# Optimization experiments

Hardware: AMD Instinct MI355X
Metric: run time of the kernel (lower is better)

## Reference

```python
import jax, jax.numpy as jnp
import numpy as np

QMIN, QMAX = -128.0, 127.0

@jax.custom_vjp
def ste_round(x):
    return jnp.round(x)

def _ste_fwd(x):
    return jnp.round(x), None

def _ste_bwd(_, g):
    return (g,)

ste_round.defvjp(_ste_fwd, _ste_bwd)

def fake_quant_act(x, scale):
    # Int8 per-tensor fake quant: q = clip(round(x/s)) * s
    return jnp.clip(ste_round(x / scale), QMIN, QMAX) * scale

def fake_quant_weight(w):
    # Int8WeightPerTensorFloat: scale from max-abs statistic
    s = jnp.max(jnp.abs(w)) / QMAX
    return jnp.clip(ste_round(w / s), QMIN, QMAX) * s

def conv2d(x, w, b, pad):
    y = jax.lax.conv_general_dilated(
        x, w, window_strides=(1, 1), padding=[(pad, pad), (pad, pad)],
        dimension_numbers=('NCHW', 'OIHW', 'NCHW'))
    return y + b[None, :, None, None]

def maxpool2(x):
    return jax.lax.reduce_window(
        x, -jnp.inf, jax.lax.max, (1, 1, 2, 2), (1, 1, 2, 2), 'VALID')

def setup_inputs() -> dict:
    key = jax.random.key(0)
    ks = jax.random.split(key, 12)
    def w_init(k, shape, fan_in):
        return jax.random.normal(k, shape, jnp.float32) * (1.0 / np.sqrt(fan_in))
    inp = {
        'x': jax.random.normal(ks[0], (32, 1, 256, 256), jnp.float32),
        'w1': w_init(ks[1], (16, 1, 3, 3), 1 * 9),
        'b1': jax.random.normal(ks[2], (16,), jnp.float32) * 0.01,
        'w2': w_init(ks[3], (32, 16, 3, 3), 16 * 9),
        'b2': jax.random.normal(ks[4], (32,), jnp.float32) * 0.01,
        'w3': w_init(ks[5], (32, 32, 5, 5), 32 * 25),
        'b3': jax.random.normal(ks[6], (32,), jnp.float32) * 0.01,
        'w4': w_init(ks[7], (16, 32, 3, 3), 32 * 9),
        'b4': jax.random.normal(ks[8], (16,), jnp.float32) * 0.01,
        'wc': w_init(ks[9], (10, 16), 16),
        'bc': jax.random.normal(ks[10], (10,), jnp.float32) * 0.01,
        # 11 learned per-tensor activation scales, kept strictly positive
        'act_scales': jax.random.uniform(ks[11], (11,), jnp.float32) * 0.05 + 0.01,
    }
    return inp

def reference(x, w1, b1, w2, b2, w3, b3, w4, b4, wc, bc, act_scales):
    s = act_scales
    x = fake_quant_act(x, s[0])                                  # input_quant
    x = conv2d(x, fake_quant_weight(w1), b1, 0)                  # conv1 (3x3, p0)
    x = fake_quant_act(jax.nn.relu(x), s[1])                     # relu1
    x = fake_quant_act(x, s[2])                                  # quant1
    x = conv2d(x, fake_quant_weight(w2), b2, 1)                  # conv2 (3x3, p1)
    x = fake_quant_act(jax.nn.relu(x), s[3])                     # relu2
    x = fake_quant_act(x, s[4])                                  # quant2
    x = conv2d(x, fake_quant_weight(w3), b3, 2)                  # conv3 (5x5, p2)
    x = fake_quant_act(jax.nn.relu(x), s[5])                     # relu3
    x = fake_quant_act(x, s[6])                                  # quant3
    x = maxpool2(x)                                              # pool1
    x = fake_quant_act(x, s[7])                                  # pool1_quant
    x = conv2d(x, fake_quant_weight(w4), b4, 0)                  # conv4 (3x3, p0)
    x = fake_quant_act(jax.nn.relu(x), s[8])                     # relu4
    x = fake_quant_act(x, s[9])                                  # quant4
    x = jnp.mean(x, axis=(2, 3))                                 # global avg pool -> [B,16]
    x = fake_quant_act(x, s[10])                                 # pool_quant
    return x @ fake_quant_weight(wc).T + bc                      # classifier -> [B,10]
```

## Files before the change

### kernel.cpp

```cpp
#include <hip/hip_runtime.h>
#include <math.h>


typedef int i32x4  __attribute__((ext_vector_type(4)));
typedef int i32x16 __attribute__((ext_vector_type(16)));

__device__ __forceinline__ int quant_clip(float v) {
  float r = rintf(v);
  r = fminf(fmaxf(r, -128.0f), 127.0f);
  return (int)r;
}

__device__ __forceinline__ int pack4i8(int q0, int q1, int q2, int q3) {
  return (q0 & 255) | ((q1 & 255) << 8) | ((q2 & 255) << 16) | ((q3 & 255) << 24);
}

__global__ __launch_bounds__(256) void k_quant_weights(
    const float* __restrict__ w1, const float* __restrict__ w2,
    const float* __restrict__ w3, const float* __restrict__ w4,
    const float* __restrict__ wc, float* __restrict__ wscale,
    int* __restrict__ qw1, int* __restrict__ qw2B, int* __restrict__ qw3B,
    int* __restrict__ qw4B, int* __restrict__ qwc)
{
  __shared__ float red[256];
  __shared__ float ssh;
  const int t = blockIdx.x, tid = threadIdx.x;
  const float* src = (t == 0) ? w1 : (t == 1) ? w2 : (t == 2) ? w3 : (t == 3) ? w4 : wc;
  const int nsrc   = (t == 0) ? 144 : (t == 1) ? 4608 : (t == 2) ? 25600 : (t == 3) ? 4608 : 160;

  float m = 0.0f;
  for (int i = tid; i < nsrc; i += 256) m = fmaxf(m, fabsf(src[i]));
  red[tid] = m;
  __syncthreads();
  for (int s = 128; s > 0; s >>= 1) {
    if (tid < s) red[tid] = fmaxf(red[tid], red[tid + s]);
    __syncthreads();
  }
  if (tid == 0) { ssh = red[0] / 127.0f; wscale[t] = ssh; }
  __syncthreads();
  const float s = ssh;

  if (t == 0) {
    for (int i = tid; i < 144; i += 256) qw1[i] = quant_clip(w1[i] / s);
  } else if (t == 1) {
    for (int wi = tid; wi < 1536; wi += 256) {
      int step = wi >> 8, rem = wi & 255;
      int ln = rem >> 2, w = rem & 3;
      int oc = ln & 31, h = ln >> 5;
      int ky = step >> 1, kxp = (step & 1) * 2;
      int q[4];
      #pragma unroll
      for (int j = 0; j < 4; j++) {
        int k = h * 16 + w * 4 + j;
        int ic = k & 15, kx = kxp + (k >> 4);
        float val = (kx < 3) ? w2[((oc * 16 + ic) * 3 + ky) * 3 + kx] : 0.0f;
        q[j] = quant_clip(val / s);
      }
      qw2B[wi] = pack4i8(q[0], q[1], q[2], q[3]);
    }
  } else if (t == 2) {
    for (int wi = tid; wi < 6400; wi += 256) {
      int tap = wi >> 8, rem = wi & 255;
      int ln = rem >> 2, w = rem & 3;
      int oc = ln & 31, h = ln >> 5;
      int ky = tap / 5, kx = tap % 5;
      int q[4];
      #pragma unroll
      for (int j = 0; j < 4; j++) {
        int ic = h * 16 + w * 4 + j;
        q[j] = quant_clip(w3[((oc * 32 + ic) * 5 + ky) * 5 + kx] / s);
      }
      qw3B[wi] = pack4i8(q[0], q[1], q[2], q[3]);
    }
  } else if (t == 3) {
    for (int wi = tid; wi < 1280; wi += 256) {
      int mf = wi >> 8, rem = wi & 255;
      int ln = rem >> 2, w = rem & 3;
      int oc = ln & 15, chunk = ln >> 4;
      int tp = 2 * mf + (chunk >> 1);
      int half = chunk & 1;
      int q[4];
      #pragma unroll
      for (int j = 0; j < 4; j++) {
        float val = 0.0f;
        if (tp < 9) {
          int ky = tp / 3, kx = tp % 3;
          int ic = half * 16 + w * 4 + j;
          val = w4[((oc * 32 + ic) * 3 + ky) * 3 + kx];
        }
        q[j] = quant_clip(val / s);
      }
      qw4B[wi] = pack4i8(q[0], q[1], q[2], q[3]);
    }
  } else {
    for (int wi = tid; wi < 40; wi += 256) {
      int o = wi / 4, i4 = wi % 4;
      int q[4];
      #pragma unroll
      for (int j = 0; j < 4; j++) q[j] = quant_clip(wc[o * 16 + i4 * 4 + j] / s);
      qwc[wi] = pack4i8(q[0], q[1], q[2], q[3]);
    }
  }
}

__global__ __launch_bounds__(256) void k_quant_input(
    const float* __restrict__ x, const float* __restrict__ scales,
    int* __restrict__ q0w)
{
  int i = blockIdx.x * 256 + threadIdx.x;
  if (i >= 524288) return;
  float inv = 1.0f / scales[0];
  float4 v = ((const float4*)x)[i];
  q0w[i] = pack4i8(quant_clip(v.x * inv), quant_clip(v.y * inv),
                   quant_clip(v.z * inv), quant_clip(v.w * inv));
}

__global__ __launch_bounds__(256) void k_zero_border(int* __restrict__ a2p)
{
  int i = blockIdx.x * 256 + threadIdx.x;
  int n = i >> 11, p = i & 2047;
  int row, col;
  if (p < 1032) {
    int rb = p / 258;
    row = (rb < 2) ? rb : 254 + rb;
    col = p % 258;
  } else {
    int q = p - 1032;
    int cb = q & 3;
    col = (cb < 2) ? cb : 254 + cb;
    row = 2 + (q >> 2);
  }
  int4* dst = (int4*)(a2p + (((size_t)n * 258 + row) * 258 + col) * 8);
  dst[0] = make_int4(0, 0, 0, 0);
  dst[1] = make_int4(0, 0, 0, 0);
}

__global__ __launch_bounds__(256) void k_conv1(
    const signed char* __restrict__ q0, const int* __restrict__ qw1,
    const float* __restrict__ b1, const float* __restrict__ scales,
    const float* __restrict__ wscale, int* __restrict__ a1)
{
  __shared__ int wsh[144];
  __shared__ signed char lut[128];
  if (threadIdx.x < 144) wsh[threadIdx.x] = qw1[threadIdx.x];
  if (threadIdx.x < 128) {
    float s1 = scales[1], inv2 = 1.0f / scales[2];
    lut[threadIdx.x] =
        (signed char)(int)fminf(rintf(((float)threadIdx.x * s1) * inv2), 127.0f);
  }
  __syncthreads();

  int pix = blockIdx.x * 256 + threadIdx.x;
  const int TOT = 32 * 254 * 254;
  if (pix >= TOT) return;
  int n = pix / (254 * 254), r = pix % (254 * 254);
  int oy = r / 254, ox = r % 254;

  int av[9];
  const signed char* base = q0 + (n * 256 + oy) * 256 + ox;
  #pragma unroll
  for (int ky = 0; ky < 3; ky++)
    #pragma unroll
    for (int kx = 0; kx < 3; kx++)
      av[ky * 3 + kx] = (int)base[ky * 256 + kx];

  float inv1 = 1.0f / scales[1];
  float scl = scales[0] * wscale[0];
  int outw[4];
  #pragma unroll
  for (int g = 0; g < 4; g++) {
    int q[4];
    #pragma unroll
    for (int j = 0; j < 4; j++) {
      int oc = g * 4 + j;
      int acc = 0;
      #pragma unroll
      for (int k = 0; k < 9; k++) acc += av[k] * wsh[oc * 9 + k];
      float y = fmaf(scl, (float)acc, b1[oc]);
      int idx = (int)fminf(fmaxf(rintf(y * inv1), 0.0f), 127.0f);
      q[j] = lut[idx];
    }
    outw[g] = pack4i8(q[0], q[1], q[2], q[3]);
  }
  *(int4*)(a1 + pix * 4) = make_int4(outw[0], outw[1], outw[2], outw[3]);
}

__global__ __launch_bounds__(256) void k_conv2_lds(
    const int* __restrict__ a1, const int* __restrict__ qw2B,
    const float* __restrict__ b2, const float* __restrict__ scales,
    const float* __restrict__ wscale, signed char* __restrict__ a2p)
{
  __shared__ __align__(16) int ash2[10 * 68 * 4];
  __shared__ signed char lut[128];

  const int tid = threadIdx.x;
  if (tid < 128) {
    float s3 = scales[3], inv4 = 1.0f / scales[4];
    lut[tid] = (signed char)(int)fminf(rintf(((float)tid * s3) * inv4), 127.0f);
  }

  const int lane = tid & 63;
  const int w = tid >> 6;
  const int bid = blockIdx.x;
  const int swz = (bid & 7) * 512 + (bid >> 3);
  const int n   = swz >> 7;
  const int rem = swz & 127;
  const int rg = rem >> 2, cg = rem & 3;
  const int r0 = rg * 8, c0 = cg * 64;

  for (int ci = tid; ci < 680; ci += 256) {
    int row = ci / 68, col = ci - row * 68;
    int gr = r0 - 1 + row, gc = c0 - 1 + col;
    i32x4 v; v[0] = 0; v[1] = 0; v[2] = 0; v[3] = 0;
    if ((unsigned)gr < 254u && (unsigned)gc < 254u)
      v = *(const i32x4*)(a1 + ((n * 254 + gr) * 254 + gc) * 4);
    *(i32x4*)&ash2[ci * 4] = v;
  }

  i32x4 bw[6];
  #pragma unroll
  for (int t = 0; t < 6; t++)
    bw[t] = *(const i32x4*)(qw2B + (t * 64 + lane) * 4);

  const float inv3 = 1.0f / scales[3];
  const float scl = scales[2] * wscale[1];
  const int oc = lane & 31, h = lane >> 5, rr = lane & 31;
  const float bias = b2[oc];

  __syncthreads();

  #pragma unroll 1
  for (int k = 0; k < 4; k++) {
    int s = k * 4 + w;
    int yl = s & 7, half = s >> 3;

    i32x4 Af[6];
    #pragma unroll
    for (int ky = 0; ky < 3; ky++) {
      #pragma unroll
      for (int kp = 0; kp < 2; kp++) {
        int srow = yl + ky;
        int scol = half * 32 + rr + kp * 2 + h;
        Af[ky * 2 + kp] = *(const i32x4*)&ash2[(srow * 68 + scol) * 4];
      }
    }

    i32x16 acc0, acc1;
    #pragma unroll
    for (int z = 0; z < 16; z++) { acc0[z] = 0; acc1[z] = 0; }
    #pragma unroll
    for (int ky = 0; ky < 3; ky++) {
      acc0 = __builtin_amdgcn_mfma_i32_32x32x32_i8(Af[ky * 2 + 0], bw[ky * 2 + 0], acc0, 0, 0, 0);
      acc1 = __builtin_amdgcn_mfma_i32_32x32x32_i8(Af[ky * 2 + 1], bw[ky * 2 + 1], acc1, 0, 0, 0);
    }

    int y = r0 + yl;
    #pragma unroll
    for (int q = 0; q < 4; q++) {
      #pragma unroll
      for (int j = 0; j < 4; j++) {
        int rowp = j + 8 * q + 4 * h;
        int x = c0 + half * 32 + rowp;
        int accv = acc0[q * 4 + j] + acc1[q * 4 + j];
        float yv = fmaf(scl, (float)accv, bias);
        int idx = (int)fminf(fmaxf(rintf(yv * inv3), 0.0f), 127.0f);
        if (x < 254 && y < 254)
          a2p[((size_t)(n * 258 + (y + 2)) * 258 + (x + 2)) * 32 + oc] =
              lut[idx];
      }
    }
  }
}

__global__ __launch_bounds__(256, 3) void k_conv3pool_mfma(
    const signed char* __restrict__ a2p, const int* __restrict__ qw3B,
    const float* __restrict__ b3, const float* __restrict__ scales,
    const float* __restrict__ wscale, signed char* __restrict__ a3p)
{
  __shared__ __align__(16) signed char ash[8 * 2176];
  __shared__ int bsh[6400];
  __shared__ signed char lut56[128];
  __shared__ signed char lut67[128];

  const int tid = threadIdx.x;
  const int lane = tid & 63;
  const int w = tid >> 6;

  const int bid = blockIdx.x;
  const int swz = (bid & 7) * 256 + (bid >> 3);
  const int n  = swz >> 6;
  const int Xg = (swz >> 4) & 3;
  const int Yq = swz & 15;
  const int c0 = 64 * Xg;

  const int oc = lane & 31, h = lane >> 5;
  const int rr = lane & 31;
  const int pp = rr >> 2, dy = (rr >> 1) & 1, dx = rr & 1;
  const int xl = 8 * w + pp;
  const int colb = (2 * xl + dx) * 32 + h * 16;
  const int X0w = 32 * Xg + 8 * w;

  const float inv5 = 1.0f / scales[5];
  const float scl = scales[4] * wscale[2];
  const float bias = b3[oc];

  {
    const int4* srcB = (const int4*)qw3B;
    int4* dstB = (int4*)bsh;
    for (int i = tid; i < 1600; i += 256) dstB[i] = srcB[i];
    if (tid < 128) {
      float s5 = scales[5], s6 = scales[6];
      float inv6 = 1.0f / s6, inv7 = 1.0f / scales[7];
      lut56[tid] = (signed char)(int)fminf(rintf(((float)tid * s5) * inv6), 127.0f);
      lut67[tid] = (signed char)(int)fminf(rintf(((float)tid * s6) * inv7), 127.0f);
    }
  }

  #pragma unroll 1
  for (int it = 0; it < 4; ++it) {
    const int Yp = 4 * Yq + it;
    const int r0 = 4 * Yp;

    __syncthreads();
    for (int ci = tid; ci < 1088; ci += 256) {
      int row = ci / 136;
      int cr = ci - row * 136;
      int col = cr >> 1, half = cr & 1;
      int gr = min(r0 + row, 257);
      int gc = min(c0 + col, 257);
      const int4* srcA = (const int4*)(a2p +
          (((size_t)n * 258 + gr) * 258 + gc) * 32 + half * 16);
      *(int4*)(&ash[row * 2176 + cr * 16]) = *srcA;
    }
    __syncthreads();

    i32x16 acc0, acc1;
    #pragma unroll
    for (int z = 0; z < 16; z++) { acc0[z] = 0; acc1[z] = 0; }

    i32x4 F0[5], F1[5], F2[5], F3[5];

#define LOAD_ROW(F, J)                                                   \
    {                                                                    \
      const signed char* rbase = &ash[(dy + (J)) * 2176 + colb];         \
      _Pragma("unroll")                                                  \
      for (int kx = 0; kx < 5; kx++)                                     \
        F[kx] = *(const i32x4*)(rbase + kx * 32);                        \
    }
#define STEP(KY, RA, RB)                                                 \
    {                                                                    \
      _Pragma("unroll")                                                  \
      for (int kx = 0; kx < 5; kx++) {                                   \
        i32x4 bfrag = *(const i32x4*)&bsh[(((KY) * 5 + kx) * 64 + lane) * 4]; \
        acc0 = __builtin_amdgcn_mfma_i32_32x32x32_i8(RA[kx], bfrag, acc0, 0, 0, 0); \
        acc1 = __builtin_amdgcn_mfma_i32_32x32x32_i8(RB[kx], bfrag, acc1, 0, 0, 0); \
      }                                                                  \
    }

    LOAD_ROW(F0, 0) LOAD_ROW(F1, 1) LOAD_ROW(F2, 2)
    LOAD_ROW(F3, 3) STEP(0, F0, F2)
    LOAD_ROW(F0, 4) STEP(1, F1, F3)
    LOAD_ROW(F1, 5) STEP(2, F2, F0)
    LOAD_ROW(F2, 6) STEP(3, F3, F1)
    STEP(4, F0, F2)
#undef LOAD_ROW
#undef STEP

    #pragma unroll
    for (int ty = 0; ty < 2; ty++) {
      int Y = 2 * Yp + ty;
      #pragma unroll
      for (int q = 0; q < 4; q++) {
        int b = 2 * q + h;
        int X = X0w + b;
        int a0, a1v, a2, a3;
        if (ty == 0) {
          a0 = acc0[q * 4 + 0]; a1v = acc0[q * 4 + 1];
          a2 = acc0[q * 4 + 2]; a3 = acc0[q * 4 + 3];
        } else {
          a0 = acc1[q * 4 + 0]; a1v = acc1[q * 4 + 1];
          a2 = acc1[q * 4 + 2]; a3 = acc1[q * 4 + 3];
        }
        int am = max(max(a0, a1v), max(a2, a3));
        float yv = fmaf(scl, (float)am, bias);
        int r1 = (int)fminf(fmaxf(rintf(yv * inv5), 0.0f), 127.0f);
        int r2 = lut56[r1];
        int r3 = lut67[r2];
        if (X < 127 && Y < 127)
          a3p[((size_t)(n * 127 + Y) * 127 + X) * 32 + oc] = (signed char)r3;
      }
    }
  }
}

__global__ __launch_bounds__(256) void k_conv4_mfma(
    const signed char* __restrict__ a3p, const int* __restrict__ qw4B,
    const float* __restrict__ b4, const float* __restrict__ scales,
    const float* __restrict__ wscale, signed char* __restrict__ a4b)
{
  __shared__ signed char lut[128];
  if (threadIdx.x < 128) {
    float s8 = scales[8], inv9 = 1.0f / scales[9];
    lut[threadIdx.x] =
        (signed char)(int)fminf(rintf(((float)threadIdx.x * s8) * inv9), 127.0f);
  }
  __syncthreads();

  const int lane = threadIdx.x & 63;
  const int bid = blockIdx.x;
  const int swz = (bid & 7) * 256 + (bid >> 3);
  const int gw = swz * 4 + (threadIdx.x >> 6);

  i32x4 bw[5];
  #pragma unroll
  for (int t = 0; t < 5; t++)
    bw[t] = *(const i32x4*)(qw4B + (t * 64 + lane) * 4);

  const int chunk = lane >> 4;
  int offB[5];
  #pragma unroll
  for (int mf = 0; mf < 5; mf++) {
    int tp = 2 * mf + (chunk >> 1);
    if (tp > 8) tp = 8;
    int ky = tp / 3, kx = tp % 3;
    offB[mf] = (ky * 127 + kx) * 32 + (chunk & 1) * 16;
  }

  const float inv8 = 1.0f / scales[8];
  const float scl = scales[7] * wscale[3];
  const int oc = lane & 15;
  const float bias = b4[oc];
  const int arow = lane & 15;

  const int TILES = 32 * 125 * 8;
  #pragma unroll 1
  for (int t4 = 0; t4 < 4; t4++) {
    int tile = gw * 4 + t4;
    if (tile >= TILES) break;
    int n = tile / 1000;
    int r = tile % 1000;
    int y = r >> 3, X0 = (r & 7) * 16;

    const signed char* base =
        a3p + ((size_t)n * 16129 + (size_t)y * 127 + (X0 + arow)) * 32;

    i32x4 Af[5];
    #pragma unroll
    for (int mf = 0; mf < 5; mf++)
      Af[mf] = *(const i32x4*)(base + offB[mf]);

    i32x4 acc;
    acc[0] = 0; acc[1] = 0; acc[2] = 0; acc[3] = 0;
    #pragma unroll
    for (int mf = 0; mf < 5; mf++)
      acc = __builtin_amdgcn_mfma_i32_16x16x64_i8(Af[mf], bw[mf], acc, 0, 0, 0);

    #pragma unroll
    for (int j = 0; j < 4; j++) {
      int x = X0 + chunk * 4 + j;
      float yv = fmaf(scl, (float)acc[j], bias);
      int idx = (int)fminf(fmaxf(rintf(yv * inv8), 0.0f), 127.0f);
      if (x < 125)
        a4b[((size_t)(n * 125 + y) * 125 + x) * 16 + oc] = lut[idx];
    }
  }
}

__global__ __launch_bounds__(256) void k_gap_stage(
    const int* __restrict__ a4, int* __restrict__ gap_acc)
{
  int img = blockIdx.x >> 4, chunk = blockIdx.x & 15;
  int tid = threadIdx.x, lane = tid & 63;
  int p0 = chunk * 977, p1 = min(p0 + 977, 15625);

  int loc[16];
  #pragma unroll
  for (int i = 0; i < 16; i++) loc[i] = 0;
  for (int p = p0 + tid; p < p1; p += 256) {
    int4 v = *(const int4*)(a4 + (img * 15625 + p) * 4);
    int w[4] = {v.x, v.y, v.z, v.w};
    #pragma unroll
    for (int wi = 0; wi < 4; wi++)
      #pragma unroll
      for (int j = 0; j < 4; j++)
        loc[wi * 4 + j] += (int)(signed char)(w[wi] >> (8 * j));
  }
  #pragma unroll
  for (int c = 0; c < 16; c++) {
    #pragma unroll
    for (int off = 32; off > 0; off >>= 1)
      loc[c] += __shfl_down(loc[c], off);
  }
  if (lane == 0) {
    #pragma unroll
    for (int c = 0; c < 16; c++) atomicAdd(&gap_acc[img * 16 + c], loc[c]);
  }
}

__global__ __launch_bounds__(64) void k_fc(
    const int* __restrict__ gap_acc, const int* __restrict__ qwc,
    const float* __restrict__ bc, const float* __restrict__ scales,
    const float* __restrict__ wscale, float* __restrict__ out)
{
  __shared__ int sq[16];
  int n = blockIdx.x, tid = threadIdx.x;
  if (tid < 16) {
    int s = gap_acc[n * 16 + tid];
    float v = scales[9] * (float)s / 15625.0f;
    float r = fminf(fmaxf(rintf(v / scales[10]), -128.0f), 127.0f);
    sq[tid] = (int)r;
  }
  __syncthreads();
  if (tid < 10) {
    int acc = 0;
    #pragma unroll
    for (int k4 = 0; k4 < 4; k4++) {
      int wv = qwc[tid * 4 + k4];
      #pragma unroll
      for (int j = 0; j < 4; j++)
        acc += sq[k4 * 4 + j] * (int)(signed char)(wv >> (8 * j));
    }
    out[n * 10 + tid] = fmaf(scales[10] * wscale[4], (float)acc, bc[tid]);
  }
}

extern "C" void kernel_launch(void* const* d_in, const int* in_sizes, int n_in,
                              void* d_out, int out_size, void* d_ws, size_t ws_size,
                              hipStream_t stream) {
  const float* x  = (const float*)d_in[0];
  const float* w1 = (const float*)d_in[1];
  const float* b1 = (const float*)d_in[2];
  const float* w2 = (const float*)d_in[3];
  const float* b2 = (const float*)d_in[4];
  const float* w3 = (const float*)d_in[5];
  const float* b3 = (const float*)d_in[6];
  const float* w4 = (const float*)d_in[7];
  const float* b4 = (const float*)d_in[8];
  const float* wc = (const float*)d_in[9];
  const float* bc = (const float*)d_in[10];
  const float* sc = (const float*)d_in[11];

  char* ws = (char*)d_ws;
  float* wscale = (float*)(ws + 0);
  int* qw1  = (int*)(ws + 64);
  int* qw2B = (int*)(ws + 1024);
  int* qw3B = (int*)(ws + 8192);
  int* qw4B = (int*)(ws + 36864);
  int* qwc  = (int*)(ws + 43008);
  int* gap_acc = (int*)(ws + 49152);
  signed char* a2p = (signed char*)(ws + 65536);
  int*  q0  = (int*)(ws + 65536);
  int*  a4  = (int*)(ws + 65536);
  int*  a1  = (int*)(ws + 68227072);
  signed char* a3p = (signed char*)(ws + 68227072);
  float* out = (float*)d_out;

  hipMemsetAsync(gap_acc, 0, 2048, stream);
  k_quant_weights<<<5, 256, 0, stream>>>(w1, w2, w3, w4, wc, wscale,
                                         qw1, qw2B, qw3B, qw4B, qwc);
  k_quant_input<<<2048, 256, 0, stream>>>(x, sc, q0);
  k_conv1<<<8065, 256, 0, stream>>>((const signed char*)q0, qw1, b1, sc, wscale, a1);
  k_zero_border<<<256, 256, 0, stream>>>((int*)a2p);
  k_conv2_lds<<<4096, 256, 0, stream>>>(a1, qw2B, b2, sc, wscale, a2p);
  k_conv3pool_mfma<<<2048, 256, 0, stream>>>(a2p, qw3B, b3, sc, wscale, a3p);
  k_conv4_mfma<<<2048, 256, 0, stream>>>(a3p, qw4B, b4, sc, wscale,
                                         (signed char*)a4);
  k_gap_stage<<<512, 256, 0, stream>>>(a4, gap_acc);
  k_fc<<<32, 64, 0, stream>>>(gap_acc, qwc, bc, sc, wscale, out);
}
```

Baseline: 276.1 us.

## Fuse input quant into conv1, GAP into conv4, swizzle LDS, parallelize weight quant

Several changes at once. Input quantization now happens inside conv1, which reads fp32 x directly, and global average pooling is folded into conv4 through shuffle reductions and atomics, so the q0 and a4 intermediate tensors are never written. An XOR swizzle is applied to LDS column indices in conv2 and conv3 to reduce bank conflicts. Weight quantization is split into a max-reduction kernel and a pack kernel spread over 40 blocks, with atomicMax on float bits. The trade-offs are that conv1 loads each input pixel 9 times as fp32 instead of int8, and conv4 now issues many small atomics.

```diff
diff --git a/kernel.cpp b/kernel.cpp
--- a/kernel.cpp
+++ b/kernel.cpp
@@ -15,35 +15,52 @@
   return (q0 & 255) | ((q1 & 255) << 8) | ((q2 & 255) << 16) | ((q3 & 255) << 24);
 }
 
-__global__ __launch_bounds__(256) void k_quant_weights(
+__device__ __forceinline__ int swz16(int c) {
+  return c ^ ((c >> 3) & 7);
+}
+
+__global__ __launch_bounds__(256) void k_wmax(
     const float* __restrict__ w1, const float* __restrict__ w2,
     const float* __restrict__ w3, const float* __restrict__ w4,
-    const float* __restrict__ wc, float* __restrict__ wscale,
-    int* __restrict__ qw1, int* __restrict__ qw2B, int* __restrict__ qw3B,
-    int* __restrict__ qw4B, int* __restrict__ qwc)
+    const float* __restrict__ wc, unsigned int* __restrict__ wsraw)
 {
   __shared__ float red[256];
-  __shared__ float ssh;
-  const int t = blockIdx.x, tid = threadIdx.x;
+  const int t = blockIdx.x >> 3, part = blockIdx.x & 7, tid = threadIdx.x;
   const float* src = (t == 0) ? w1 : (t == 1) ? w2 : (t == 2) ? w3 : (t == 3) ? w4 : wc;
-  const int nsrc   = (t == 0) ? 144 : (t == 1) ? 4608 : (t == 2) ? 25600 : (t == 3) ? 4608 : 160;
+  const int n4 = (t == 0) ? 36 : (t == 1) ? 1152 : (t == 2) ? 6400 : (t == 3) ? 1152 : 40;
 
   float m = 0.0f;
-  for (int i = tid; i < nsrc; i += 256) m = fmaxf(m, fabsf(src[i]));
+  for (int i = part * 256 + tid; i < n4; i += 2048) {
+    float4 v = ((const float4*)src)[i];
+    m = fmaxf(m, fmaxf(fmaxf(fabsf(v.x), fabsf(v.y)),
+                       fmaxf(fabsf(v.z), fabsf(v.w))));
+  }
   red[tid] = m;
   __syncthreads();
   for (int s = 128; s > 0; s >>= 1) {
     if (tid < s) red[tid] = fmaxf(red[tid], red[tid + s]);
     __syncthreads();
   }
-  if (tid == 0) { ssh = red[0] / 127.0f; wscale[t] = ssh; }
-  __syncthreads();
-  const float s = ssh;
+  if (tid == 0) atomicMax(&wsraw[t], __float_as_uint(red[0]));
+}
+
+__global__ __launch_bounds__(256) void k_wpack(
+    const float* __restrict__ w1, const float* __restrict__ w2,
+    const float* __restrict__ w3, const float* __restrict__ w4,
+    const float* __restrict__ wc, const unsigned int* __restrict__ wsraw,
+    float* __restrict__ wscale,
+    int* __restrict__ qw1, int* __restrict__ qw2B, int* __restrict__ qw3B,
+    int* __restrict__ qw4B, int* __restrict__ qwc)
+{
+  const int t = blockIdx.x >> 3, part = blockIdx.x & 7, tid = threadIdx.x;
+  const float s = __uint_as_float(wsraw[t]) / 127.0f;
+  if (part == 0 && tid == 0) wscale[t] = s;
+  const int base = part * 256 + tid;
 
   if (t == 0) {
-    for (int i = tid; i < 144; i += 256) qw1[i] = quant_clip(w1[i] / s);
+    for (int i = base; i < 144; i += 2048) qw1[i] = quant_clip(w1[i] / s);
   } else if (t == 1) {
-    for (int wi = tid; wi < 1536; wi += 256) {
+    for (int wi = base; wi < 1536; wi += 2048) {
       int step = wi >> 8, rem = wi & 255;
       int ln = rem >> 2, w = rem & 3;
       int oc = ln & 31, h = ln >> 5;
@@ -59,7 +76,7 @@
       qw2B[wi] = pack4i8(q[0], q[1], q[2], q[3]);
     }
   } else if (t == 2) {
-    for (int wi = tid; wi < 6400; wi += 256) {
+    for (int wi = base; wi < 6400; wi += 2048) {
       int tap = wi >> 8, rem = wi & 255;
       int ln = rem >> 2, w = rem & 3;
       int oc = ln & 31, h = ln >> 5;
@@ -73,7 +90,7 @@
       qw3B[wi] = pack4i8(q[0], q[1], q[2], q[3]);
     }
   } else if (t == 3) {
-    for (int wi = tid; wi < 1280; wi += 256) {
+    for (int wi = base; wi < 1280; wi += 2048) {
       int mf = wi >> 8, rem = wi & 255;
       int ln = rem >> 2, w = rem & 3;
       int oc = ln & 15, chunk = ln >> 4;
@@ -93,7 +110,7 @@
       qw4B[wi] = pack4i8(q[0], q[1], q[2], q[3]);
     }
   } else {
-    for (int wi = tid; wi < 40; wi += 256) {
+    for (int wi = base; wi < 40; wi += 2048) {
       int o = wi / 4, i4 = wi % 4;
       int q[4];
       #pragma unroll
@@ -101,18 +118,6 @@
       qwc[wi] = pack4i8(q[0], q[1], q[2], q[3]);
     }
   }
-}
-
-__global__ __launch_bounds__(256) void k_quant_input(
-    const float* __restrict__ x, const float* __restrict__ scales,
-    int* __restrict__ q0w)
-{
-  int i = blockIdx.x * 256 + threadIdx.x;
-  if (i >= 524288) return;
-  float inv = 1.0f / scales[0];
-  float4 v = ((const float4*)x)[i];
-  q0w[i] = pack4i8(quant_clip(v.x * inv), quant_clip(v.y * inv),
-                   quant_clip(v.z * inv), quant_clip(v.w * inv));
 }
 
 __global__ __launch_bounds__(256) void k_zero_border(int* __restrict__ a2p)
@@ -136,7 +141,7 @@
 }
 
 __global__ __launch_bounds__(256) void k_conv1(
-    const signed char* __restrict__ q0, const int* __restrict__ qw1,
+    const float* __restrict__ x, const int* __restrict__ qw1,
     const float* __restrict__ b1, const float* __restrict__ scales,
     const float* __restrict__ wscale, int* __restrict__ a1)
 {
@@ -156,13 +161,14 @@
   int n = pix / (254 * 254), r = pix % (254 * 254);
   int oy = r / 254, ox = r % 254;
 
+  float inv0 = 1.0f / scales[0];
   int av[9];
-  const signed char* base = q0 + (n * 256 + oy) * 256 + ox;
+  const float* base = x + (n * 256 + oy) * 256 + ox;
   #pragma unroll
   for (int ky = 0; ky < 3; ky++)
     #pragma unroll
     for (int kx = 0; kx < 3; kx++)
-      av[ky * 3 + kx] = (int)base[ky * 256 + kx];
+      av[ky * 3 + kx] = quant_clip(base[ky * 256 + kx] * inv0);
 
   float inv1 = 1.0f / scales[1];
   float scl = scales[0] * wscale[0];
@@ -214,7 +220,7 @@
     i32x4 v; v[0] = 0; v[1] = 0; v[2] = 0; v[3] = 0;
     if ((unsigned)gr < 254u && (unsigned)gc < 254u)
       v = *(const i32x4*)(a1 + ((n * 254 + gr) * 254 + gc) * 4);
-    *(i32x4*)&ash2[ci * 4] = v;
+    *(i32x4*)&ash2[(row * 68 + swz16(col)) * 4] = v;
   }
 
   i32x4 bw[6];
@@ -241,7 +247,7 @@
       for (int kp = 0; kp < 2; kp++) {
         int srow = yl + ky;
         int scol = half * 32 + rr + kp * 2 + h;
-        Af[ky * 2 + kp] = *(const i32x4*)&ash2[(srow * 68 + scol) * 4];
+        Af[ky * 2 + kp] = *(const i32x4*)&ash2[(srow * 68 + swz16(scol)) * 4];
       }
     }
 
@@ -287,18 +293,24 @@
   const int w = tid >> 6;
 
   const int bid = blockIdx.x;
-  const int swz = (bid & 7) * 256 + (bid >> 3);
-  const int n  = swz >> 6;
-  const int Xg = (swz >> 4) & 3;
-  const int Yq = swz & 15;
+  const int swzb = (bid & 7) * 256 + (bid >> 3);
+  const int n  = swzb >> 6;
+  const int Xg = (swzb >> 4) & 3;
+  const int Yq = swzb & 15;
   const int c0 = 64 * Xg;
 
   const int oc = lane & 31, h = lane >> 5;
   const int rr = lane & 31;
   const int pp = rr >> 2, dy = (rr >> 1) & 1, dx = rr & 1;
   const int xl = 8 * w + pp;
-  const int colb = (2 * xl + dx) * 32 + h * 16;
   const int X0w = 32 * Xg + 8 * w;
+
+  int csw[5];
+  {
+    int c0l = 4 * xl + 2 * dx + h;
+    #pragma unroll
+    for (int kx = 0; kx < 5; kx++) csw[kx] = swz16(c0l + 2 * kx) * 16;
+  }
 
   const float inv5 = 1.0f / scales[5];
   const float scl = scales[4] * wscale[2];
@@ -330,7 +342,7 @@
       int gc = min(c0 + col, 257);
       const int4* srcA = (const int4*)(a2p +
           (((size_t)n * 258 + gr) * 258 + gc) * 32 + half * 16);
-      *(int4*)(&ash[row * 2176 + cr * 16]) = *srcA;
+      *(int4*)(&ash[row * 2176 + swz16(cr) * 16]) = *srcA;
     }
     __syncthreads();
 
@@ -342,10 +354,10 @@
 
 #define LOAD_ROW(F, J)                                                   \
     {                                                                    \
-      const signed char* rbase = &ash[(dy + (J)) * 2176 + colb];         \
+      const signed char* rbase = &ash[(dy + (J)) * 2176];                \
       _Pragma("unroll")                                                  \
       for (int kx = 0; kx < 5; kx++)                                     \
-        F[kx] = *(const i32x4*)(rbase + kx * 32);                        \
+        F[kx] = *(const i32x4*)(rbase + csw[kx]);                        \
     }
 #define STEP(KY, RA, RB)                                                 \
     {                                                                    \
@@ -393,10 +405,10 @@
   }
 }
 
-__global__ __launch_bounds__(256) void k_conv4_mfma(
+__global__ __launch_bounds__(256) void k_conv4_gap(
     const signed char* __restrict__ a3p, const int* __restrict__ qw4B,
     const float* __restrict__ b4, const float* __restrict__ scales,
-    const float* __restrict__ wscale, signed char* __restrict__ a4b)
+    const float* __restrict__ wscale, int* __restrict__ gap_acc)
 {
   __shared__ signed char lut[128];
   if (threadIdx.x < 128) {
@@ -455,45 +467,17 @@
     for (int mf = 0; mf < 5; mf++)
       acc = __builtin_amdgcn_mfma_i32_16x16x64_i8(Af[mf], bw[mf], acc, 0, 0, 0);
 
+    int ssum = 0;
     #pragma unroll
     for (int j = 0; j < 4; j++) {
       int x = X0 + chunk * 4 + j;
       float yv = fmaf(scl, (float)acc[j], bias);
       int idx = (int)fminf(fmaxf(rintf(yv * inv8), 0.0f), 127.0f);
-      if (x < 125)
-        a4b[((size_t)(n * 125 + y) * 125 + x) * 16 + oc] = lut[idx];
-    }
-  }
-}
-
-__global__ __launch_bounds__(256) void k_gap_stage(
-    const int* __restrict__ a4, int* __restrict__ gap_acc)
-{
-  int img = blockIdx.x >> 4, chunk = blockIdx.x & 15;
-  int tid = threadIdx.x, lane = tid & 63;
-  int p0 = chunk * 977, p1 = min(p0 + 977, 15625);
-
-  int loc[16];
-  #pragma unroll
-  for (int i = 0; i < 16; i++) loc[i] = 0;
-  for (int p = p0 + tid; p < p1; p += 256) {
-    int4 v = *(const int4*)(a4 + (img * 15625 + p) * 4);
-    int w[4] = {v.x, v.y, v.z, v.w};
-    #pragma unroll
-    for (int wi = 0; wi < 4; wi++)
-      #pragma unroll
-      for (int j = 0; j < 4; j++)
-        loc[wi * 4 + j] += (int)(signed char)(w[wi] >> (8 * j));
-  }
-  #pragma unroll
-  for (int c = 0; c < 16; c++) {
-    #pragma unroll
-    for (int off = 32; off > 0; off >>= 1)
-      loc[c] += __shfl_down(loc[c], off);
-  }
-  if (lane == 0) {
-    #pragma unroll
-    for (int c = 0; c < 16; c++) atomicAdd(&gap_acc[img * 16 + c], loc[c]);
+      if (x < 125) ssum += lut[idx];
+    }
+    ssum += __shfl_down(ssum, 32);
+    ssum += __shfl_down(ssum, 16);
+    if (lane < 16) atomicAdd(&gap_acc[n * 16 + oc], ssum);
   }
 }
 
@@ -548,23 +532,20 @@
   int* qw4B = (int*)(ws + 36864);
   int* qwc  = (int*)(ws + 43008);
   int* gap_acc = (int*)(ws + 49152);
+  unsigned int* wsraw = (unsigned int*)(ws + 51200);
   signed char* a2p = (signed char*)(ws + 65536);
-  int*  q0  = (int*)(ws + 65536);
-  int*  a4  = (int*)(ws + 65536);
   int*  a1  = (int*)(ws + 68227072);
   signed char* a3p = (signed char*)(ws + 68227072);
   float* out = (float*)d_out;
 
-  hipMemsetAsync(gap_acc, 0, 2048, stream);
-  k_quant_weights<<<5, 256, 0, stream>>>(w1, w2, w3, w4, wc, wscale,
-                                         qw1, qw2B, qw3B, qw4B, qwc);
-  k_quant_input<<<2048, 256, 0, stream>>>(x, sc, q0);
-  k_conv1<<<8065, 256, 0, stream>>>((const signed char*)q0, qw1, b1, sc, wscale, a1);
+  hipMemsetAsync(ws + 49152, 0, 4096, stream);
+  k_wmax<<<40, 256, 0, stream>>>(w1, w2, w3, w4, wc, wsraw);
+  k_wpack<<<40, 256, 0, stream>>>(w1, w2, w3, w4, wc, wsraw, wscale,
+                                  qw1, qw2B, qw3B, qw4B, qwc);
+  k_conv1<<<8065, 256, 0, stream>>>(x, qw1, b1, sc, wscale, a1);
   k_zero_border<<<256, 256, 0, stream>>>((int*)a2p);
   k_conv2_lds<<<4096, 256, 0, stream>>>(a1, qw2B, b2, sc, wscale, a2p);
   k_conv3pool_mfma<<<2048, 256, 0, stream>>>(a2p, qw3B, b3, sc, wscale, a3p);
-  k_conv4_mfma<<<2048, 256, 0, stream>>>(a3p, qw4B, b4, sc, wscale,
-                                         (signed char*)a4);
-  k_gap_stage<<<512, 256, 0, stream>>>(a4, gap_acc);
+  k_conv4_gap<<<2048, 256, 0, stream>>>(a3p, qw4B, b4, sc, wscale, gap_acc);
   k_fc<<<32, 64, 0, stream>>>(gap_acc, qwc, bc, sc, wscale, out);
 }
```

Result: faster. 252.1 us (-8.7%).
